# Kernel tuning notes

Hardware: AMD Instinct MI355X
Metric: run time of the kernel (lower is better)

Reference implementation:

```python
import jax, jax.numpy as jnp
import numpy as np

S = 8192      # s: number of persons/nodes
F = 1024      # feature_len
A = 256       # attn_len
SIGMA_X, SIGMA_Y = 4.0, 1.0
EPS_VALID = 1e-8
EPS_DIS = 1e-4


def setup_inputs() -> dict:
    key = jax.random.key(0)
    ks = jax.random.split(key, 8)
    batch_data = jax.random.normal(ks[0], (S, F), dtype=jnp.float32)
    xywh = jax.random.uniform(ks[1], (S, 4), dtype=jnp.float32)  # positive -> all rows valid
    actor_weights = jax.random.uniform(ks[2], (S,), dtype=jnp.float32)
    avg_pos = jax.random.uniform(ks[3], (S, 2), dtype=jnp.float32)
    # learned params (kaiming-ish init, zero bias as in original)
    W_h = jax.random.normal(ks[4], (F, 2), dtype=jnp.float32) * (2.0 / F) ** 0.5
    b_h = jnp.zeros((2,), dtype=jnp.float32)
    W_g = jax.random.normal(ks[5], (F, A), dtype=jnp.float32) * (2.0 / F) ** 0.5
    b_g = jnp.zeros((A,), dtype=jnp.float32)
    return {
        "batch_data": batch_data, "xywh": xywh, "OW": 1920, "OH": 1080,
        "actor_weights": actor_weights, "avg_pos": avg_pos,
        "W_h": W_h, "b_h": b_h, "W_g": W_g, "b_g": b_g, "num_person": S,
    }


def reference(batch_data, xywh, OW, OH, actor_weights, avg_pos, W_h, b_h, W_g, b_g, num_person):
    # highlight_fc + tanh -> predicted offsets [S,2]
    hp = jnp.tanh(batch_data @ W_h + b_h)
    hx = hp[:, 0] * xywh[:, 2] * SIGMA_X + xywh[:, 0]  # [S]
    hy = hp[:, 1] * xywh[:, 3] * SIGMA_Y + xywh[:, 1]  # [S]

    # gcn_fc + relu -> node messages [S,A]
    targets = jax.nn.relu(batch_data @ W_g + b_g)

    # valid rows/cols: torch loop skips i/j with sum(xywh) < 1e-8
    valid = jnp.sum(xywh, axis=1) >= EPS_VALID  # [S] bool

    # pairwise inverse-distance weights [S,S] (the memory-bound core)
    dx = hx[:, None] - xywh[None, :, 0]
    dy = hy[:, None] - xywh[None, :, 1]
    dis = jnp.sqrt(dx * dx + dy * dy)
    pair_valid = valid[:, None] & valid[None, :]
    w = jnp.where(pair_valid, 1.0 / (dis + EPS_DIS), 0.0)
    row_sum = jnp.sum(w, axis=1, keepdims=True)
    w = jnp.where(valid[:, None], w / jnp.maximum(row_sum, 1e-30), 0.0)

    targets_weighted = w @ targets  # [S,A]
    return (targets_weighted, hp)
```

## Files before the change

### kernel.cpp

```cpp
#include <hip/hip_runtime.h>
#include <math.h>
#include <stdint.h>

typedef __attribute__((ext_vector_type(8))) short short8;
typedef __attribute__((ext_vector_type(4))) float f32x4;

__device__ __forceinline__ uint32_t cvt_pk_bf16(float lo, float hi) {
  uint32_t r;
  asm("v_cvt_pk_bf16_f32 %0, %1, %2" : "=v"(r) : "v"(lo), "v"(hi));
  return r;
}

__device__ __forceinline__ float wfun(float hx, float hy, float cx, float cy) {
  float dx = hx - cx, dy = hy - cy;
  float d = __builtin_amdgcn_sqrtf(fmaf(dx, dx, dy * dy));
  return __builtin_amdgcn_rcpf(d + 1e-4f);
}

__global__ __launch_bounds__(256) void k_prep_w(
    const float* __restrict__ Wg, uint16_t* __restrict__ WgT, int F, int A) {
  int idx = blockIdx.x * 256 + threadIdx.x;
  int a = idx % A;
  int k0 = (idx / A) * 8;
  if (k0 >= F) return;
  float f[8];
  #pragma unroll
  for (int e = 0; e < 8; ++e) f[e] = Wg[(size_t)(k0 + e) * A + a];
  uint4 v;
  v.x = cvt_pk_bf16(f[0], f[1]);
  v.y = cvt_pk_bf16(f[2], f[3]);
  v.z = cvt_pk_bf16(f[4], f[5]);
  v.w = cvt_pk_bf16(f[6], f[7]);
  *(uint4*)(WgT + (size_t)a * F + k0) = v;
}

__global__ __launch_bounds__(256) void k_fused_tgt_head(
    const float* __restrict__ batch, const uint16_t* __restrict__ WgT,
    const float* __restrict__ bg, const float* __restrict__ W_h,
    const float* __restrict__ b_h, const float* __restrict__ xywh,
    uint16_t* __restrict__ tgt2, float* __restrict__ hp_out,
    float* __restrict__ hx, float* __restrict__ hy,
    float* __restrict__ validf, float2* __restrict__ cxy,
    int S, int F, int A) {
  int t = threadIdx.x;
  int lane = t & 63, wid = t >> 6;
  int wm = wid >> 1, wn = wid & 1;
  int i0 = blockIdx.x * 32;
  int row = i0 + wm * 16 + (lane & 15);
  int kch = lane >> 4;
  const float* ab = batch + (size_t)row * F + kch * 8;
  int ncol0 = wn * 128 + (lane & 15);
  const uint16_t* bb = WgT + (size_t)ncol0 * F + kch * 8;

  f32x4 acc[8] = {};
  float wh0 = 0.f, wh1 = 0.f;
  float4 a0 = *(const float4*)(ab);
  float4 a1 = *(const float4*)(ab + 4);
  short8 bf[8];
  #pragma unroll
  for (int nf = 0; nf < 8; ++nf)
    bf[nf] = *(const short8*)(bb + (size_t)nf * 16 * F);

  for (int k0 = 0; k0 < F; k0 += 32) {
    int kn = (k0 + 32 < F) ? k0 + 32 : 0;
    float4 na0 = *(const float4*)(ab + kn);
    float4 na1 = *(const float4*)(ab + kn + 4);
    short8 nbf[8];
    #pragma unroll
    for (int nf = 0; nf < 8; ++nf)
      nbf[nf] = *(const short8*)(bb + kn + (size_t)nf * 16 * F);

    if (wn == 0) {
      const float* whp = W_h + 2 * (k0 + kch * 8);
      float4 h0 = *(const float4*)(whp);
      float4 h1 = *(const float4*)(whp + 4);
      float4 h2 = *(const float4*)(whp + 8);
      float4 h3 = *(const float4*)(whp + 12);
      wh0 += a0.x*h0.x + a0.y*h0.z + a0.z*h1.x + a0.w*h1.z
           + a1.x*h2.x + a1.y*h2.z + a1.z*h3.x + a1.w*h3.z;
      wh1 += a0.x*h0.y + a0.y*h0.w + a0.z*h1.y + a0.w*h1.w
           + a1.x*h2.y + a1.y*h2.w + a1.z*h3.y + a1.w*h3.w;
    }

    union { short8 s; uint32_t u[4]; } af;
    af.u[0] = cvt_pk_bf16(a0.x, a0.y);
    af.u[1] = cvt_pk_bf16(a0.z, a0.w);
    af.u[2] = cvt_pk_bf16(a1.x, a1.y);
    af.u[3] = cvt_pk_bf16(a1.z, a1.w);
    #pragma unroll
    for (int nf = 0; nf < 8; ++nf)
      acc[nf] = __builtin_amdgcn_mfma_f32_16x16x32_bf16(af.s, bf[nf], acc[nf], 0, 0, 0);
    a0 = na0; a1 = na1;
    #pragma unroll
    for (int nf = 0; nf < 8; ++nf) bf[nf] = nbf[nf];
  }

  int jb = blockIdx.x;
  int rloc = wm * 16 + (lane >> 4) * 4;
  #pragma unroll
  for (int nf = 0; nf < 8; ++nf) {
    int col = ncol0 + nf * 16;
    float b = bg[col];
    float o0 = fmaxf(acc[nf][0] + b, 0.f);
    float o1 = fmaxf(acc[nf][1] + b, 0.f);
    float o2 = fmaxf(acc[nf][2] + b, 0.f);
    float o3 = fmaxf(acc[nf][3] + b, 0.f);
    uint2 pk;
    pk.x = cvt_pk_bf16(o0, o1);
    pk.y = cvt_pk_bf16(o2, o3);
    *(uint2*)(tgt2 + ((size_t)jb * A + col) * 32 + rloc) = pk;
  }

  if (wn == 0) {
    wh0 += __shfl_xor(wh0, 16, 64);
    wh0 += __shfl_xor(wh0, 32, 64);
    wh1 += __shfl_xor(wh1, 16, 64);
    wh1 += __shfl_xor(wh1, 32, 64);
    if (lane < 16) {
      int r = i0 + wm * 16 + lane;
      float hp0 = tanhf(wh0 + b_h[0]);
      float hp1 = tanhf(wh1 + b_h[1]);
      float4 xy = ((const float4*)xywh)[r];
      hp_out[2 * r] = hp0;
      hp_out[2 * r + 1] = hp1;
      hx[r] = hp0 * xy.z * 4.0f + xy.x;
      hy[r] = hp1 * xy.w * 1.0f + xy.y;
      bool v = (xy.x + xy.y + xy.z + xy.w >= 1e-8f);
      validf[r] = v ? 1.0f : 0.0f;
      cxy[r] = v ? make_float2(xy.x, xy.y) : make_float2(1e30f, 1e30f);
    }
  }
}

__global__ __launch_bounds__(1024, 4) void k_gather_v16(
    const uint16_t* __restrict__ tgt2, const float2* __restrict__ cxy,
    const float* __restrict__ hx, const float* __restrict__ hy,
    const float* __restrict__ validf, float* __restrict__ out, int S, int A) {
  __shared__ uint16_t Bt[2][2][256][40];
  __shared__ uint32_t Af[2][2][2][64][4];
  __shared__ float comb[32][260];
  __shared__ float rs_l[2][32][16];
  __shared__ float scale_s[32];

  int t = threadIdx.x;
  int lane = t & 63, wid = t >> 6;
  int kg = wid >> 3;
  int sub = wid & 7;
  int wm = sub >> 2, wn = sub & 3;
  int i0 = blockIdx.x * 32;
  int kch = lane >> 4;
  int n0 = wn * 64 + (lane & 15);
  int NT = (S >> 1) / 32;
  const size_t TSTRIDE = (size_t)A * 32;
  const int COLS = 40;

  int u = t & 511;
  int wr = u & 31;
  int wjp = u >> 5;
  float hx_w = hx[i0 + wr], hy_w = hy[i0 + wr];
  uint32_t* afw0 = &Af[0][kg][wr >> 4][(wr & 15) | ((wjp >> 2) << 4)][wjp & 3];
  uint32_t* afw1 = &Af[1][kg][wr >> 4][(wr & 15) | ((wjp >> 2) << 4)][wjp & 3];
  const float2* gC = cxy + (size_t)kg * (S >> 1) + 2 * wjp;

  int scol = u >> 1;
  int skw = u & 1;
  const uint16_t* gB0 = tgt2 + (size_t)(kg * NT) * TSTRIDE
                        + (size_t)scol * 32 + skw * 16;

  f32x4 acc[4] = {};
  float rs = 0.f;

  {
    float4 c0 = *(const float4*)(gC);
    float wA = wfun(hx_w, hy_w, c0.x, c0.y);
    float wB = wfun(hx_w, hy_w, c0.z, c0.w);
    rs += wA + wB;
    *afw0 = cvt_pk_bf16(wA, wB);
    uint4 ga = *(const uint4*)(gB0);
    uint4 gb = *(const uint4*)(gB0 + 8);
    *(uint4*)&Bt[0][kg][scol][skw * 16] = ga;
    *(uint4*)&Bt[0][kg][scol][skw * 16 + 8] = gb;
  }
  float4 ccur = *(const float4*)(gC + 32);
  __syncthreads();

  for (int ts = 0; ts < NT; ++ts) {
    int nxt = (ts & 1) ^ 1;
    int tn = (ts + 1 < NT) ? ts + 1 : 0;
    int tf = (ts + 2 < NT) ? ts + 2 : 0;

    const uint16_t* bp = gB0 + (size_t)tn * TSTRIDE;
    uint4 ga = *(const uint4*)(bp);
    uint4 gb = *(const uint4*)(bp + 8);
    float4 cfut = *(const float4*)(gC + (size_t)tf * 32);

    const uint32_t* afp = &Af[ts & 1][kg][wm][lane][0];
    short8 afr = *(const short8*)afp;
    const uint16_t* br = &Bt[ts & 1][kg][n0][kch * 8];
    short8 b0 = *(const short8*)(br);
    short8 b1 = *(const short8*)(br + 16 * COLS);
    short8 b2 = *(const short8*)(br + 32 * COLS);
    short8 b3 = *(const short8*)(br + 48 * COLS);

    acc[0] = __builtin_amdgcn_mfma_f32_16x16x32_bf16(afr, b0, acc[0], 0, 0, 0);
    acc[1] = __builtin_amdgcn_mfma_f32_16x16x32_bf16(afr, b1, acc[1], 0, 0, 0);
    acc[2] = __builtin_amdgcn_mfma_f32_16x16x32_bf16(afr, b2, acc[2], 0, 0, 0);
    acc[3] = __builtin_amdgcn_mfma_f32_16x16x32_bf16(afr, b3, acc[3], 0, 0, 0);

    float wA = wfun(hx_w, hy_w, ccur.x, ccur.y);
    float wB = wfun(hx_w, hy_w, ccur.z, ccur.w);
    float g = (ts + 1 < NT) ? 1.f : 0.f;
    rs = fmaf(g, wA + wB, rs);
    uint32_t pk = cvt_pk_bf16(wA, wB);
    uint32_t* afw = nxt ? afw1 : afw0;
    *afw = pk;

    *(uint4*)&Bt[nxt][kg][scol][skw * 16] = ga;
    *(uint4*)&Bt[nxt][kg][scol][skw * 16 + 8] = gb;
    ccur = cfut;
    __syncthreads();
  }

  rs_l[kg][wr][wjp] = rs;

  if (kg == 1) {
    int mre = wm * 16 + (lane >> 4) * 4;
    #pragma unroll
    for (int r = 0; r < 4; ++r) {
      comb[mre + r][n0]      = acc[0][r];
      comb[mre + r][n0 + 16] = acc[1][r];
      comb[mre + r][n0 + 32] = acc[2][r];
      comb[mre + r][n0 + 48] = acc[3][r];
    }
  }
  __syncthreads();
  if (t < 32) {
    float r = 0.f;
    #pragma unroll
    for (int jp = 0; jp < 16; ++jp) r += rs_l[0][t][jp] + rs_l[1][t][jp];
    float v = validf[i0 + t];
    scale_s[t] = (v > 0.f) ? 1.0f / fmaxf(r, 1e-30f) : 0.f;
  }
  __syncthreads();
  if (kg == 0) {
    int mre = wm * 16 + (lane >> 4) * 4;
    #pragma unroll
    for (int r = 0; r < 4; ++r) {
      float s = scale_s[mre + r];
      size_t base = (size_t)(i0 + mre + r) * A;
      out[base + n0]      = (acc[0][r] + comb[mre + r][n0]) * s;
      out[base + n0 + 16] = (acc[1][r] + comb[mre + r][n0 + 16]) * s;
      out[base + n0 + 32] = (acc[2][r] + comb[mre + r][n0 + 32]) * s;
      out[base + n0 + 48] = (acc[3][r] + comb[mre + r][n0 + 48]) * s;
    }
  }
}

extern "C" void kernel_launch(void* const* d_in, const int* in_sizes, int n_in,
                              void* d_out, int out_size, void* d_ws, size_t ws_size,
                              hipStream_t stream) {
  const float* batch = (const float*)d_in[0];
  const float* xywh  = (const float*)d_in[1];
  const float* W_h   = (const float*)d_in[6];
  const float* b_h   = (const float*)d_in[7];
  const float* W_g   = (const float*)d_in[8];
  const float* b_g   = (const float*)d_in[9];
  int S = in_sizes[4];
  int F = in_sizes[0] / S;
  int A = in_sizes[9];

  float* out    = (float*)d_out;
  float* out_tw = out;
  float* out_hp = out + (size_t)S * A;

  uint16_t* tgt2 = (uint16_t*)d_ws;
  uint16_t* WgT  = tgt2 + (size_t)A * S;
  float* hxv = (float*)(WgT + (size_t)A * F);
  float* hyv = hxv + S;
  float* vfv = hyv + S;
  float2* cxyv = (float2*)(vfv + S);

  k_prep_w<<<dim3((A * F / 8 + 255) / 256), 256, 0, stream>>>(W_g, WgT, F, A);
  k_fused_tgt_head<<<dim3(S / 32), 256, 0, stream>>>(batch, WgT, b_g, W_h, b_h,
                                                     xywh, tgt2, out_hp, hxv,
                                                     hyv, vfv, cxyv, S, F, A);
  k_gather_v16<<<dim3(S / 32), 1024, 0, stream>>>(tgt2, cxyv, hxv, hyv, vfv,
                                                  out_tw, S, A);
}
```

Measured before the change: 142.9 us.

## Retile gather GEMM to 64 rows x 128 cols with 4-way K split

The gather kernel now has each block handle 64 output rows by half of the 256 columns. The K dimension is split four ways instead of two, and each wave computes two 16-row M tiles that share the same B fragments. This raises reuse of each loaded B tile and halves the number of row tiles. In exchange, every block recomputes the distance weights for its rows, since the two column halves both need them. The four K-group partial sums are then combined through shared memory in several serialized synchronized steps.

Result: faster. 131.9 us (median of 2 runs) (-7.8%).

```diff
diff --git a/kernel.cpp b/kernel.cpp
--- a/kernel.cpp
+++ b/kernel.cpp
@@ -132,126 +132,232 @@
   }
 }
 
-__global__ __launch_bounds__(1024, 4) void k_gather_v16(
+__global__ __launch_bounds__(1024, 4) void k_gather_v20(
     const uint16_t* __restrict__ tgt2, const float2* __restrict__ cxy,
     const float* __restrict__ hx, const float* __restrict__ hy,
     const float* __restrict__ validf, float* __restrict__ out, int S, int A) {
-  __shared__ uint16_t Bt[2][2][256][40];
-  __shared__ uint32_t Af[2][2][2][64][4];
-  __shared__ float comb[32][260];
-  __shared__ float rs_l[2][32][16];
-  __shared__ float scale_s[32];
+  __shared__ uint16_t Bt[2][4][128][40];
+  __shared__ uint32_t Af[2][4][2][2][64][4];
+  __shared__ float comb[64][132];
+  __shared__ float rs_l[4][64][4];
+  __shared__ float scale_s[64];
 
   int t = threadIdx.x;
   int lane = t & 63, wid = t >> 6;
-  int kg = wid >> 3;
-  int sub = wid & 7;
-  int wm = sub >> 2, wn = sub & 3;
-  int i0 = blockIdx.x * 32;
+  int kg = wid >> 2;
+  int sub = wid & 3;
+  int wm = sub >> 1, wn = sub & 1;
+  int colhalf = blockIdx.x;
+  int i0 = blockIdx.y * 64;
   int kch = lane >> 4;
   int n0 = wn * 64 + (lane & 15);
-  int NT = (S >> 1) / 32;
+  int NT = S / (4 * 32);
   const size_t TSTRIDE = (size_t)A * 32;
   const int COLS = 40;
 
-  int u = t & 511;
-  int wr = u & 31;
-  int wjp = u >> 5;
+  int wkg = t >> 8;
+  int v = t & 255;
+  int wr = v & 63;
+  int z = v >> 6;
+  int m2 = (z & 1) * 2;
+  int h0 = z >> 1;
   float hx_w = hx[i0 + wr], hy_w = hy[i0 + wr];
-  uint32_t* afw0 = &Af[0][kg][wr >> 4][(wr & 15) | ((wjp >> 2) << 4)][wjp & 3];
-  uint32_t* afw1 = &Af[1][kg][wr >> 4][(wr & 15) | ((wjp >> 2) << 4)][wjp & 3];
-  const float2* gC = cxy + (size_t)kg * (S >> 1) + 2 * wjp;
-
-  int scol = u >> 1;
-  int skw = u & 1;
-  const uint16_t* gB0 = tgt2 + (size_t)(kg * NT) * TSTRIDE
-                        + (size_t)scol * 32 + skw * 16;
-
-  f32x4 acc[4] = {};
+  int rgw = wr >> 5, wmw = (wr >> 4) & 1, rl = wr & 15;
+  uint32_t* afA0 = &Af[0][wkg][wmw][rgw][rl | (h0 << 4)][m2];
+  uint32_t* afB0 = &Af[0][wkg][wmw][rgw][rl | ((h0 + 2) << 4)][m2];
+  uint32_t* afA1 = &Af[1][wkg][wmw][rgw][rl | (h0 << 4)][m2];
+  uint32_t* afB1 = &Af[1][wkg][wmw][rgw][rl | ((h0 + 2) << 4)][m2];
+  const float2* gC = cxy + (size_t)wkg * (S >> 2);
+  int cOffA = 8 * h0 + 2 * m2;
+  int cOffB = cOffA + 16;
+
+  int scol = v >> 1;
+  int skw = v & 1;
+  const uint16_t* gB0 = tgt2 + (size_t)(wkg * NT) * TSTRIDE
+                        + (size_t)(colhalf * 128 + scol) * 32 + skw * 16;
+
+  f32x4 acc0[4] = {};
+  f32x4 acc1[4] = {};
   float rs = 0.f;
 
   {
-    float4 c0 = *(const float4*)(gC);
-    float wA = wfun(hx_w, hy_w, c0.x, c0.y);
-    float wB = wfun(hx_w, hy_w, c0.z, c0.w);
-    rs += wA + wB;
-    *afw0 = cvt_pk_bf16(wA, wB);
     uint4 ga = *(const uint4*)(gB0);
     uint4 gb = *(const uint4*)(gB0 + 8);
-    *(uint4*)&Bt[0][kg][scol][skw * 16] = ga;
-    *(uint4*)&Bt[0][kg][scol][skw * 16 + 8] = gb;
-  }
-  float4 ccur = *(const float4*)(gC + 32);
+    *(uint4*)&Bt[0][wkg][scol][skw * 16] = ga;
+    *(uint4*)&Bt[0][wkg][scol][skw * 16 + 8] = gb;
+    float4 ca = *(const float4*)(gC + cOffA);
+    float4 cb = *(const float4*)(gC + cOffA + 2);
+    float4 cc = *(const float4*)(gC + cOffB);
+    float4 cd = *(const float4*)(gC + cOffB + 2);
+    float w0 = wfun(hx_w, hy_w, ca.x, ca.y);
+    float w1 = wfun(hx_w, hy_w, ca.z, ca.w);
+    float w2 = wfun(hx_w, hy_w, cb.x, cb.y);
+    float w3 = wfun(hx_w, hy_w, cb.z, cb.w);
+    float w4 = wfun(hx_w, hy_w, cc.x, cc.y);
+    float w5 = wfun(hx_w, hy_w, cc.z, cc.w);
+    float w6 = wfun(hx_w, hy_w, cd.x, cd.y);
+    float w7 = wfun(hx_w, hy_w, cd.z, cd.w);
+    rs += ((w0 + w1) + (w2 + w3)) + ((w4 + w5) + (w6 + w7));
+    uint2 pA = make_uint2(cvt_pk_bf16(w0, w1), cvt_pk_bf16(w2, w3));
+    uint2 pB = make_uint2(cvt_pk_bf16(w4, w5), cvt_pk_bf16(w6, w7));
+    *(uint2*)afA0 = pA;
+    *(uint2*)afB0 = pB;
+  }
   __syncthreads();
 
   for (int ts = 0; ts < NT; ++ts) {
-    int nxt = (ts & 1) ^ 1;
+    int cur = ts & 1, nxt = cur ^ 1;
     int tn = (ts + 1 < NT) ? ts + 1 : 0;
-    int tf = (ts + 2 < NT) ? ts + 2 : 0;
 
     const uint16_t* bp = gB0 + (size_t)tn * TSTRIDE;
     uint4 ga = *(const uint4*)(bp);
     uint4 gb = *(const uint4*)(bp + 8);
-    float4 cfut = *(const float4*)(gC + (size_t)tf * 32);
-
-    const uint32_t* afp = &Af[ts & 1][kg][wm][lane][0];
-    short8 afr = *(const short8*)afp;
-    const uint16_t* br = &Bt[ts & 1][kg][n0][kch * 8];
+    const float2* cp = gC + (size_t)tn * 32;
+    float4 ca = *(const float4*)(cp + cOffA);
+    float4 cb = *(const float4*)(cp + cOffA + 2);
+    float4 cc = *(const float4*)(cp + cOffB);
+    float4 cd = *(const float4*)(cp + cOffB + 2);
+
+    short8 a0 = *(const short8*)&Af[cur][kg][wm][0][lane][0];
+    short8 a1 = *(const short8*)&Af[cur][kg][wm][1][lane][0];
+    const uint16_t* br = &Bt[cur][kg][n0][kch * 8];
     short8 b0 = *(const short8*)(br);
     short8 b1 = *(const short8*)(br + 16 * COLS);
     short8 b2 = *(const short8*)(br + 32 * COLS);
     short8 b3 = *(const short8*)(br + 48 * COLS);
 
-    acc[0] = __builtin_amdgcn_mfma_f32_16x16x32_bf16(afr, b0, acc[0], 0, 0, 0);
-    acc[1] = __builtin_amdgcn_mfma_f32_16x16x32_bf16(afr, b1, acc[1], 0, 0, 0);
-    acc[2] = __builtin_amdgcn_mfma_f32_16x16x32_bf16(afr, b2, acc[2], 0, 0, 0);
-    acc[3] = __builtin_amdgcn_mfma_f32_16x16x32_bf16(afr, b3, acc[3], 0, 0, 0);
-
-    float wA = wfun(hx_w, hy_w, ccur.x, ccur.y);
-    float wB = wfun(hx_w, hy_w, ccur.z, ccur.w);
+    acc0[0] = __builtin_amdgcn_mfma_f32_16x16x32_bf16(a0, b0, acc0[0], 0, 0, 0);
+    acc0[1] = __builtin_amdgcn_mfma_f32_16x16x32_bf16(a0, b1, acc0[1], 0, 0, 0);
+    acc0[2] = __builtin_amdgcn_mfma_f32_16x16x32_bf16(a0, b2, acc0[2], 0, 0, 0);
+    acc0[3] = __builtin_amdgcn_mfma_f32_16x16x32_bf16(a0, b3, acc0[3], 0, 0, 0);
+    acc1[0] = __builtin_amdgcn_mfma_f32_16x16x32_bf16(a1, b0, acc1[0], 0, 0, 0);
+    acc1[1] = __builtin_amdgcn_mfma_f32_16x16x32_bf16(a1, b1, acc1[1], 0, 0, 0);
+    acc1[2] = __builtin_amdgcn_mfma_f32_16x16x32_bf16(a1, b2, acc1[2], 0, 0, 0);
+    acc1[3] = __builtin_amdgcn_mfma_f32_16x16x32_bf16(a1, b3, acc1[3], 0, 0, 0);
+
+    float w0 = wfun(hx_w, hy_w, ca.x, ca.y);
+    float w1 = wfun(hx_w, hy_w, ca.z, ca.w);
+    float w2 = wfun(hx_w, hy_w, cb.x, cb.y);
+    float w3 = wfun(hx_w, hy_w, cb.z, cb.w);
+    float w4 = wfun(hx_w, hy_w, cc.x, cc.y);
+    float w5 = wfun(hx_w, hy_w, cc.z, cc.w);
+    float w6 = wfun(hx_w, hy_w, cd.x, cd.y);
+    float w7 = wfun(hx_w, hy_w, cd.z, cd.w);
     float g = (ts + 1 < NT) ? 1.f : 0.f;
-    rs = fmaf(g, wA + wB, rs);
-    uint32_t pk = cvt_pk_bf16(wA, wB);
-    uint32_t* afw = nxt ? afw1 : afw0;
-    *afw = pk;
-
-    *(uint4*)&Bt[nxt][kg][scol][skw * 16] = ga;
-    *(uint4*)&Bt[nxt][kg][scol][skw * 16 + 8] = gb;
-    ccur = cfut;
+    rs = fmaf(g, ((w0 + w1) + (w2 + w3)) + ((w4 + w5) + (w6 + w7)), rs);
+    uint2 pA = make_uint2(cvt_pk_bf16(w0, w1), cvt_pk_bf16(w2, w3));
+    uint2 pB = make_uint2(cvt_pk_bf16(w4, w5), cvt_pk_bf16(w6, w7));
+    *(uint2*)(nxt ? afA1 : afA0) = pA;
+    *(uint2*)(nxt ? afB1 : afB0) = pB;
+
+    *(uint4*)&Bt[nxt][wkg][scol][skw * 16] = ga;
+    *(uint4*)&Bt[nxt][wkg][scol][skw * 16 + 8] = gb;
     __syncthreads();
   }
 
-  rs_l[kg][wr][wjp] = rs;
+  rs_l[wkg][wr][z] = rs;
+  int rbase = (lane >> 4) * 4;
 
   if (kg == 1) {
-    int mre = wm * 16 + (lane >> 4) * 4;
-    #pragma unroll
-    for (int r = 0; r < 4; ++r) {
-      comb[mre + r][n0]      = acc[0][r];
-      comb[mre + r][n0 + 16] = acc[1][r];
-      comb[mre + r][n0 + 32] = acc[2][r];
-      comb[mre + r][n0 + 48] = acc[3][r];
-    }
-  }
-  __syncthreads();
-  if (t < 32) {
+    #pragma unroll
+    for (int r = 0; r < 4; ++r) {
+      int r0 = wm * 16 + rbase + r, r1 = 32 + r0;
+      comb[r0][n0]      = acc0[0][r];
+      comb[r0][n0 + 16] = acc0[1][r];
+      comb[r0][n0 + 32] = acc0[2][r];
+      comb[r0][n0 + 48] = acc0[3][r];
+      comb[r1][n0]      = acc1[0][r];
+      comb[r1][n0 + 16] = acc1[1][r];
+      comb[r1][n0 + 32] = acc1[2][r];
+      comb[r1][n0 + 48] = acc1[3][r];
+    }
+  }
+  __syncthreads();
+  if (t < 64) {
     float r = 0.f;
     #pragma unroll
-    for (int jp = 0; jp < 16; ++jp) r += rs_l[0][t][jp] + rs_l[1][t][jp];
-    float v = validf[i0 + t];
-    scale_s[t] = (v > 0.f) ? 1.0f / fmaxf(r, 1e-30f) : 0.f;
-  }
-  __syncthreads();
+    for (int k2 = 0; k2 < 4; ++k2)
+      #pragma unroll
+      for (int z2 = 0; z2 < 4; ++z2) r += rs_l[k2][t][z2];
+    float fv = validf[i0 + t];
+    scale_s[t] = (fv > 0.f) ? 1.0f / fmaxf(r, 1e-30f) : 0.f;
+  }
   if (kg == 0) {
-    int mre = wm * 16 + (lane >> 4) * 4;
-    #pragma unroll
-    for (int r = 0; r < 4; ++r) {
-      float s = scale_s[mre + r];
-      size_t base = (size_t)(i0 + mre + r) * A;
-      out[base + n0]      = (acc[0][r] + comb[mre + r][n0]) * s;
-      out[base + n0 + 16] = (acc[1][r] + comb[mre + r][n0 + 16]) * s;
-      out[base + n0 + 32] = (acc[2][r] + comb[mre + r][n0 + 32]) * s;
-      out[base + n0 + 48] = (acc[3][r] + comb[mre + r][n0 + 48]) * s;
+    #pragma unroll
+    for (int r = 0; r < 4; ++r) {
+      int r0 = wm * 16 + rbase + r, r1 = 32 + r0;
+      acc0[0][r] += comb[r0][n0];
+      acc0[1][r] += comb[r0][n0 + 16];
+      acc0[2][r] += comb[r0][n0 + 32];
+      acc0[3][r] += comb[r0][n0 + 48];
+      acc1[0][r] += comb[r1][n0];
+      acc1[1][r] += comb[r1][n0 + 16];
+      acc1[2][r] += comb[r1][n0 + 32];
+      acc1[3][r] += comb[r1][n0 + 48];
+    }
+  }
+  __syncthreads();
+  if (kg == 2) {
+    #pragma unroll
+    for (int r = 0; r < 4; ++r) {
+      int r0 = wm * 16 + rbase + r, r1 = 32 + r0;
+      comb[r0][n0]      = acc0[0][r];
+      comb[r0][n0 + 16] = acc0[1][r];
+      comb[r0][n0 + 32] = acc0[2][r];
+      comb[r0][n0 + 48] = acc0[3][r];
+      comb[r1][n0]      = acc1[0][r];
+      comb[r1][n0 + 16] = acc1[1][r];
+      comb[r1][n0 + 32] = acc1[2][r];
+      comb[r1][n0 + 48] = acc1[3][r];
+    }
+  }
+  __syncthreads();
+  if (kg == 0) {
+    #pragma unroll
+    for (int r = 0; r < 4; ++r) {
+      int r0 = wm * 16 + rbase + r, r1 = 32 + r0;
+      acc0[0][r] += comb[r0][n0];
+      acc0[1][r] += comb[r0][n0 + 16];
+      acc0[2][r] += comb[r0][n0 + 32];
+      acc0[3][r] += comb[r0][n0 + 48];
+      acc1[0][r] += comb[r1][n0];
+      acc1[1][r] += comb[r1][n0 + 16];
+      acc1[2][r] += comb[r1][n0 + 32];
+      acc1[3][r] += comb[r1][n0 + 48];
+    }
+  }
+  __syncthreads();
+  if (kg == 3) {
+    #pragma unroll
+    for (int r = 0; r < 4; ++r) {
+      int r0 = wm * 16 + rbase + r, r1 = 32 + r0;
+      comb[r0][n0]      = acc0[0][r];
+      comb[r0][n0 + 16] = acc0[1][r];
+      comb[r0][n0 + 32] = acc0[2][r];
+      comb[r0][n0 + 48] = acc0[3][r];
+      comb[r1][n0]      = acc1[0][r];
+      comb[r1][n0 + 16] = acc1[1][r];
+      comb[r1][n0 + 32] = acc1[2][r];
+      comb[r1][n0 + 48] = acc1[3][r];
+    }
+  }
+  __syncthreads();
+  if (kg == 0) {
+    int cb = colhalf * 128;
+    #pragma unroll
+    for (int r = 0; r < 4; ++r) {
+      int r0 = wm * 16 + rbase + r, r1 = 32 + r0;
+      float s0 = scale_s[r0], s1 = scale_s[r1];
+      size_t b0o = (size_t)(i0 + r0) * A + cb;
+      size_t b1o = (size_t)(i0 + r1) * A + cb;
+      out[b0o + n0]      = (acc0[0][r] + comb[r0][n0]) * s0;
+      out[b0o + n0 + 16] = (acc0[1][r] + comb[r0][n0 + 16]) * s0;
+      out[b0o + n0 + 32] = (acc0[2][r] + comb[r0][n0 + 32]) * s0;
+      out[b0o + n0 + 48] = (acc0[3][r] + comb[r0][n0 + 48]) * s0;
+      out[b1o + n0]      = (acc1[0][r] + comb[r1][n0]) * s1;
+      out[b1o + n0 + 16] = (acc1[1][r] + comb[r1][n0 + 16]) * s1;
+      out[b1o + n0 + 32] = (acc1[2][r] + comb[r1][n0 + 32]) * s1;
+      out[b1o + n0 + 48] = (acc1[3][r] + comb[r1][n0 + 48]) * s1;
     }
   }
 }
@@ -284,6 +390,6 @@
   k_fused_tgt_head<<<dim3(S / 32), 256, 0, stream>>>(batch, WgT, b_g, W_h, b_h,
                                                      xywh, tgt2, out_hp, hxv,
                                                      hyv, vfv, cxyv, S, F, A);
-  k_gather_v16<<<dim3(S / 32), 1024, 0, stream>>>(tgt2, cxyv, hxv, hyv, vfv,
-                                                  out_tw, S, A);
-}
+  k_gather_v20<<<dim3(2, S / 64), 1024, 0, stream>>>(tgt2, cxyv, hxv, hyv, vfv,
+                                                     out_tw, S, A);
+}
```
